# Optimization experiments

Hardware: AMD Instinct MI355X
Metric: run time of the kernel (lower is better)

## Reference

```python
import jax, jax.numpy as jnp
import numpy as np

B, E, N1, K, CIN, CB, COUT, G = 2, 2048, 96, 32, 64, 32, 64, 4
NEG_SLOPE = 0.01  # nn.LeakyReLU default


def setup_inputs() -> dict:
    key = jax.random.key(0)
    ks = jax.random.split(key, 9)
    sites1 = jax.random.normal(ks[0], (B, N1, CIN), jnp.float32)
    sites2 = jax.random.normal(ks[1], (B, K, CIN), jnp.float32)
    bonds = jax.random.normal(ks[2], (B, E, CB), jnp.float32)
    idx1 = jax.random.randint(ks[3], (E,), 0, N1, jnp.int32)
    idx2 = jax.random.randint(ks[4], (E,), 0, K, jnp.int32)
    idx2_oh = jax.nn.one_hot(idx2, K, dtype=jnp.float32)  # [E, K]
    F = 2 * CIN + CB
    W_eq = jax.random.normal(ks[5], (G, F, COUT), jnp.float32) / np.float32(np.sqrt(F))
    b_eq = jnp.zeros((COUT,), jnp.float32)
    W_att = jax.random.normal(ks[6], (COUT, 1), jnp.float32) / np.float32(np.sqrt(COUT))
    b_att = jnp.zeros((1,), jnp.float32)
    # permutation group action on the K cells: identity + random perms
    perms = [jnp.arange(K, dtype=jnp.int32)]
    pk = ks[7]
    for _ in range(G - 1):
        pk, sk = jax.random.split(pk)
        perms.append(jax.random.permutation(sk, K).astype(jnp.int32))
    perms1 = jnp.stack(perms)  # [G, K]
    perms2 = perms1            # same action on input and output cell axes
    return dict(sites1=sites1, sites2=sites2, bonds=bonds, W_eq=W_eq, b_eq=b_eq,
                W_att=W_att, b_att=b_att, idx2_oh=idx2_oh, idx1=idx1, idx2=idx2,
                perms1=perms1, perms2=perms2)


def reference(sites1, sites2, bonds, W_eq, b_eq, W_att, b_att, idx2_oh, idx1, idx2, perms1, perms2):
    Bn = sites1.shape[0]
    Gn, Kn = perms1.shape
    On = W_eq.shape[2]
    # gather sender / receiver site features along the site axis
    sites_s = jnp.take(sites1, idx1, axis=1)              # [B,E,CIN]
    sites_r = jnp.take(sites2, idx2, axis=1)              # [B,E,CIN]
    vectors = jnp.concatenate([sites_s, sites_r, bonds], axis=2)  # [B,E,F]
    # outer-product expansion onto cells (idx2_oh is one-hot over K)
    vc = jnp.einsum('bef,ek->befk', vectors, idx2_oh)     # [B,E,F,K]
    # permutation-equivariant linear (group-averaged): per-group-element weight,
    # input cells permuted by perms1, output cells un-permuted by perms2
    xg = vc[:, :, :, perms1]                               # [B,E,F,G,K]
    yg = jnp.einsum('befgk,gfo->beogk', xg, W_eq)          # [B,E,O,G,K]
    inv2 = jnp.argsort(perms2, axis=1)                     # inverse perms [G,K]
    garr = jnp.arange(Gn)[:, None]
    y = yg[:, :, :, garr, inv2].mean(axis=3)               # [B,E,O,K]
    y = jax.nn.leaky_relu(y + b_eq[None, None, :, None], NEG_SLOPE)
    # gather each edge's receiving cell slot == dot with one-hot
    lat = jnp.einsum('beok,ek->beo', y, idx2_oh)           # [B,E,O]
    att = jax.nn.sigmoid(jnp.einsum('beo,oj->bej', lat, W_att) + b_att)  # [B,E,1]
    lat = att * lat
    # scatter_add over edges into receiving sites
    out = jnp.zeros((Bn, Kn, On), lat.dtype).at[:, idx2].add(lat)  # [B,K,O]
    return out
```

## Files before the change

### kernel.cpp

```cpp
#include <hip/hip_runtime.h>
#include <math.h>

#define Bn   2
#define En   2048
#define N1n  96
#define Kn   32
#define CINn 64
#define CBn  32
#define On   64
#define Gn   4
#define Fn   160
#define NEG  0.01f
#define NW   8
#define NT   (NW * 64)
#define EB   2
#define SUBn 8
#define ELCAP 128

__global__ void __launch_bounds__(NT, 4)
fused_kernel(const float* __restrict__ sites1, const float* __restrict__ sites2,
             const float* __restrict__ bonds,  const float* __restrict__ W_eq,
             const float* __restrict__ b_eq,   const float* __restrict__ W_att,
             const float* __restrict__ b_att,  const int* __restrict__ idx1,
             const int* __restrict__ idx2,     const int* __restrict__ perms1,
             const int* __restrict__ perms2,   float* __restrict__ ws) {
    __shared__ float Weff[Fn][On];
    __shared__ float vs[NW][EB][96];
    __shared__ float red[NW][On];
    __shared__ float s2[CINn];
    __shared__ float wgs[Gn];
    __shared__ int   elist[ELCAP];
    __shared__ int   ecount;

    const int t      = threadIdx.x;
    const int bucket = blockIdx.x >> 3;
    const int sub    = blockIdx.x & (SUBn - 1);
    const int b      = bucket >> 5;
    const int k2     = bucket & (Kn - 1);

    if (t < Gn) wgs[t] = 0.f;
    __builtin_amdgcn_wave_barrier();
    if (t < 64) {
        const int pa2 = perms2[t],      pa1 = perms1[t];
        const int pb2 = perms2[t + 64], pb1 = perms1[t + 64];
        if (pa2 == k2 && pa1 == k2) wgs[t >> 5] = 1.f;
        if (pb2 == k2 && pb1 == k2) wgs[(t + 64) >> 5] = 1.f;
    }
    if (t == 64) ecount = 0;
    __syncthreads();

    for (int e = t; e < En; e += NT)
        if (idx2[e] == k2 && (e & (SUBn - 1)) == sub) {
            int p = atomicAdd(&ecount, 1);
            elist[p] = e;
        }

    {
        const float w0 = wgs[0], w1 = wgs[1], w2 = wgs[2], w3 = wgs[3];
        const float4* W4 = (const float4*)W_eq;
        float4* Wd = (float4*)&Weff[0][0];
        const int n4 = Fn * On / 4;
#pragma unroll
        for (int i = t; i < n4; i += NT) {
            float4 a0 = W4[i], a1 = W4[n4 + i], a2 = W4[2 * n4 + i], a3 = W4[3 * n4 + i];
            float4 r;
            r.x = 0.25f * (w0 * a0.x + w1 * a1.x + w2 * a2.x + w3 * a3.x);
            r.y = 0.25f * (w0 * a0.y + w1 * a1.y + w2 * a2.y + w3 * a3.y);
            r.z = 0.25f * (w0 * a0.z + w1 * a1.z + w2 * a2.z + w3 * a3.z);
            r.w = 0.25f * (w0 * a0.w + w1 * a1.w + w2 * a2.w + w3 * a3.w);
            Wd[i] = r;
        }
    }

    if (t < CINn) s2[t] = sites2[(b * Kn + k2) * CINn + t];
    __syncthreads();

    const int w    = t >> 6;
    const int lane = t & 63;
    const int og   = lane & 15;
    const int fg   = lane >> 4;
    const int ec   = ecount;

    const float4 be4 = ((const float4*)b_eq)[og];
    const float4 wa  = ((const float4*)W_att)[og];
    const float  ba  = b_att[0];

    float4 p2 = make_float4(0.f, 0.f, 0.f, 0.f);
#pragma unroll
    for (int fi = 0; fi < 16; ++fi) {
        const int f  = 64 + 4 * fi + fg;
        const float  vf = s2[4 * fi + fg];
        const float4 wv = *(const float4*)&Weff[f][og * 4];
        p2.x += vf * wv.x; p2.y += vf * wv.y;
        p2.z += vf * wv.z; p2.w += vf * wv.w;
    }

    float4 oacc = make_float4(0.f, 0.f, 0.f, 0.f);

    for (int base = w * EB; base < ec; base += NW * EB) {
        const int nb = (ec - base < EB) ? (ec - base) : EB;

        __builtin_amdgcn_wave_barrier();
#pragma unroll
        for (int j = 0; j < EB; ++j) {
            const int jj = j < nb ? j : nb - 1;
            const int e  = elist[base + jj];
            const int i1 = idx1[e];
            vs[w][j][lane] = sites1[((b * N1n + i1) << 6) + lane];
            if (lane < CBn) vs[w][j][CINn + lane] = bonds[(b * En + e) * CBn + lane];
        }
        __builtin_amdgcn_wave_barrier();

        float4 acc[EB];
#pragma unroll
        for (int j = 0; j < EB; ++j) acc[j] = p2;

#pragma unroll
        for (int fi = 0; fi < 24; ++fi) {
            const int vsidx = 4 * fi + fg;
            const int f     = vsidx < CINn ? vsidx : vsidx + CINn;
            const float4 wv = *(const float4*)&Weff[f][og * 4];
#pragma unroll
            for (int j = 0; j < EB; ++j) {
                const float vf = vs[w][j][vsidx];
                acc[j].x += vf * wv.x; acc[j].y += vf * wv.y;
                acc[j].z += vf * wv.z; acc[j].w += vf * wv.w;
            }
        }
        __builtin_amdgcn_wave_barrier();

#pragma unroll
        for (int j = 0; j < EB; ++j) {
            float4 a = acc[j];
#pragma unroll
            for (int m = 16; m <= 32; m <<= 1) {
                a.x += __shfl_xor(a.x, m);
                a.y += __shfl_xor(a.y, m);
                a.z += __shfl_xor(a.z, m);
                a.w += __shfl_xor(a.w, m);
            }
            float4 lat;
            lat.x = a.x + be4.x; lat.x = lat.x > 0.f ? lat.x : NEG * lat.x;
            lat.y = a.y + be4.y; lat.y = lat.y > 0.f ? lat.y : NEG * lat.y;
            lat.z = a.z + be4.z; lat.z = lat.z > 0.f ? lat.z : NEG * lat.z;
            lat.w = a.w + be4.w; lat.w = lat.w > 0.f ? lat.w : NEG * lat.w;

            float part = lat.x * wa.x + lat.y * wa.y + lat.z * wa.z + lat.w * wa.w;
#pragma unroll
            for (int m = 1; m <= 8; m <<= 1) part += __shfl_xor(part, m);

            float att = 1.f / (1.f + expf(-(part + ba)));
            att *= (j < nb) ? 1.f : 0.f;
            oacc.x += att * lat.x;
            oacc.y += att * lat.y;
            oacc.z += att * lat.z;
            oacc.w += att * lat.w;
        }
    }

    if (fg == 0) *(float4*)&red[w][og * 4] = oacc;
    __syncthreads();

    if (t < On) {
        float s = 0.f;
#pragma unroll
        for (int q = 0; q < NW; ++q) s += red[q][t];
        ws[((size_t)bucket * SUBn + sub) * On + t] = s;
    }
}

__global__ void __launch_bounds__(256)
reduce_kernel(const float* __restrict__ ws, float* __restrict__ out) {
    const int i = blockIdx.x * 256 + threadIdx.x;
    const int bucket = i >> 6;
    const int o      = i & (On - 1);
    const float* p = ws + (size_t)bucket * SUBn * On + o;
    float s01 = p[0]      + p[On];
    float s23 = p[2 * On] + p[3 * On];
    float s45 = p[4 * On] + p[5 * On];
    float s67 = p[6 * On] + p[7 * On];
    out[i] = (s01 + s23) + (s45 + s67);
}

extern "C" void kernel_launch(void* const* d_in, const int* in_sizes, int n_in,
                              void* d_out, int out_size, void* d_ws, size_t ws_size,
                              hipStream_t stream) {
    const float* sites1 = (const float*)d_in[0];
    const float* sites2 = (const float*)d_in[1];
    const float* bonds  = (const float*)d_in[2];
    const float* W_eq   = (const float*)d_in[3];
    const float* b_eq   = (const float*)d_in[4];
    const float* W_att  = (const float*)d_in[5];
    const float* b_att  = (const float*)d_in[6];
    const int*   idx1   = (const int*)d_in[8];
    const int*   idx2   = (const int*)d_in[9];
    const int*   perms1 = (const int*)d_in[10];
    const int*   perms2 = (const int*)d_in[11];
    float* out = (float*)d_out;
    float* ws  = (float*)d_ws;

    fused_kernel<<<Bn * Kn * SUBn, NT, 0, stream>>>(
        sites1, sites2, bonds, W_eq, b_eq, W_att, b_att,
        idx1, idx2, perms1, perms2, ws);
    reduce_kernel<<<(Bn * Kn * On) / 256, 256, 0, stream>>>(ws, out);
}
```

Baseline: 84.58 us.

## Precompute per-cell weights and edge lists in prep kernel; fuse final reduction via ticket

A new prep kernel builds the group-averaged weight matrix once per receiving cell, rather than once in every one of the 512 blocks, and builds each cell's edge list once in global workspace. The main kernel copies the precomputed weights into shared memory and takes a contiguous slice of the edge list. The separate reduce kernel is replaced by a last-block-done atomic ticket that sums the partials inside the main kernel. This removes redundant W_eq reads and per-block idx2 scans at the cost of an extra launch and workspace traffic. Two risks: edges beyond 160 per cell are dropped, and the ticket counters are reset only for t<64, which covers all 64 buckets.

```diff
diff --git a/kernel.cpp b/kernel.cpp
--- a/kernel.cpp
+++ b/kernel.cpp
@@ -15,53 +15,40 @@
 #define NT   (NW * 64)
 #define EB   2
 #define SUBn 8
-#define ELCAP 128
-
-__global__ void __launch_bounds__(NT, 4)
-fused_kernel(const float* __restrict__ sites1, const float* __restrict__ sites2,
-             const float* __restrict__ bonds,  const float* __restrict__ W_eq,
-             const float* __restrict__ b_eq,   const float* __restrict__ W_att,
-             const float* __restrict__ b_att,  const int* __restrict__ idx1,
-             const int* __restrict__ idx2,     const int* __restrict__ perms1,
-             const int* __restrict__ perms2,   float* __restrict__ ws) {
-    __shared__ float Weff[Fn][On];
-    __shared__ float vs[NW][EB][96];
-    __shared__ float red[NW][On];
-    __shared__ float s2[CINn];
-    __shared__ float wgs[Gn];
-    __shared__ int   elist[ELCAP];
-    __shared__ int   ecount;
-
-    const int t      = threadIdx.x;
-    const int bucket = blockIdx.x >> 3;
-    const int sub    = blockIdx.x & (SUBn - 1);
-    const int b      = bucket >> 5;
-    const int k2     = bucket & (Kn - 1);
-
-    if (t < Gn) wgs[t] = 0.f;
-    __builtin_amdgcn_wave_barrier();
-    if (t < 64) {
-        const int pa2 = perms2[t],      pa1 = perms1[t];
-        const int pb2 = perms2[t + 64], pb1 = perms1[t + 64];
-        if (pa2 == k2 && pa1 == k2) wgs[t >> 5] = 1.f;
-        if (pb2 == k2 && pb1 == k2) wgs[(t + 64) >> 5] = 1.f;
-    }
-    if (t == 64) ecount = 0;
-    __syncthreads();
-
-    for (int e = t; e < En; e += NT)
-        if (idx2[e] == k2 && (e & (SUBn - 1)) == sub) {
-            int p = atomicAdd(&ecount, 1);
-            elist[p] = e;
-        }
-
-    {
+#define LCAP 160
+
+#define WS_TICK 0
+#define WS_CNT  64
+#define WS_LIST 256
+#define WS_WEFF 8192
+#define WS_PART (8192 + 32 * Fn * On)
+
+__global__ void __launch_bounds__(NT)
+prep_kernel(const float* __restrict__ W_eq, const int* __restrict__ perms1,
+            const int* __restrict__ perms2, const int* __restrict__ idx2,
+            float* __restrict__ wsf) {
+    int* wsi = (int*)wsf;
+    const int t    = threadIdx.x;
+    const int role = blockIdx.x;
+
+    if (role < 64) {
+        const int k2 = role >> 1;
+        __shared__ float wgs[Gn];
+        if (t < Gn) wgs[t] = 0.f;
+        __builtin_amdgcn_wave_barrier();
+        if (t < 64) {
+            const int pa2 = perms2[t],      pa1 = perms1[t];
+            const int pb2 = perms2[t + 64], pb1 = perms1[t + 64];
+            if (pa2 == k2 && pa1 == k2) wgs[t >> 5] = 1.f;
+            if (pb2 == k2 && pb1 == k2) wgs[(t + 64) >> 5] = 1.f;
+        }
+        __syncthreads();
         const float w0 = wgs[0], w1 = wgs[1], w2 = wgs[2], w3 = wgs[3];
         const float4* W4 = (const float4*)W_eq;
-        float4* Wd = (float4*)&Weff[0][0];
+        float4* Wd = (float4*)(wsf + WS_WEFF + k2 * (Fn * On));
         const int n4 = Fn * On / 4;
-#pragma unroll
-        for (int i = t; i < n4; i += NT) {
+        const int i0 = (role & 1) * (n4 / 2);
+        for (int i = i0 + t; i < i0 + n4 / 2; i += NT) {
             float4 a0 = W4[i], a1 = W4[n4 + i], a2 = W4[2 * n4 + i], a3 = W4[3 * n4 + i];
             float4 r;
             r.x = 0.25f * (w0 * a0.x + w1 * a1.x + w2 * a2.x + w3 * a3.x);
@@ -70,8 +57,54 @@
             r.w = 0.25f * (w0 * a0.w + w1 * a1.w + w2 * a2.w + w3 * a3.w);
             Wd[i] = r;
         }
-    }
-
+    } else {
+        const int k2 = role - 64;
+        __shared__ int cntS;
+        if (t == 0) cntS = 0;
+        if (role == 64 && t < 64) wsi[WS_TICK + t] = 0;
+        __syncthreads();
+        for (int e = t; e < En; e += NT)
+            if (idx2[e] == k2) {
+                int p = atomicAdd(&cntS, 1);
+                if (p < LCAP) wsi[WS_LIST + k2 * LCAP + p] = e;
+            }
+        __syncthreads();
+        if (t == 0) wsi[WS_CNT + k2] = cntS < LCAP ? cntS : LCAP;
+    }
+}
+
+__global__ void __launch_bounds__(NT, 4)
+fused_kernel(const float* __restrict__ sites1, const float* __restrict__ sites2,
+             const float* __restrict__ bonds,  const float* __restrict__ b_eq,
+             const float* __restrict__ W_att,  const float* __restrict__ b_att,
+             const int* __restrict__ idx1,     float* __restrict__ wsf,
+             float* __restrict__ out) {
+    __shared__ float Weff[Fn][On];
+    __shared__ float vs[NW][EB][96];
+    __shared__ float red[NW][On];
+    __shared__ float s2[CINn];
+    __shared__ int   el[64];
+    __shared__ int   s_last;
+
+    int* wsi = (int*)wsf;
+    const int t      = threadIdx.x;
+    const int bucket = blockIdx.x >> 3;
+    const int sub    = blockIdx.x & (SUBn - 1);
+    const int b      = bucket >> 5;
+    const int k2     = bucket & (Kn - 1);
+
+    const int c  = wsi[WS_CNT + k2];
+    const int ch = (c + SUBn - 1) >> 3;
+    const int lo = sub * ch;
+    int n = c - lo; if (n > ch) n = ch; if (n < 0) n = 0;
+    if (t < n) el[t] = wsi[WS_LIST + k2 * LCAP + lo + t];
+
+    {
+        const float4* Ws4 = (const float4*)(wsf + WS_WEFF + k2 * (Fn * On));
+        float4* Wd = (float4*)&Weff[0][0];
+#pragma unroll
+        for (int i = t; i < Fn * On / 4; i += NT) Wd[i] = Ws4[i];
+    }
     if (t < CINn) s2[t] = sites2[(b * Kn + k2) * CINn + t];
     __syncthreads();
 
@@ -79,7 +112,6 @@
     const int lane = t & 63;
     const int og   = lane & 15;
     const int fg   = lane >> 4;
-    const int ec   = ecount;
 
     const float4 be4 = ((const float4*)b_eq)[og];
     const float4 wa  = ((const float4*)W_att)[og];
@@ -97,14 +129,14 @@
 
     float4 oacc = make_float4(0.f, 0.f, 0.f, 0.f);
 
-    for (int base = w * EB; base < ec; base += NW * EB) {
-        const int nb = (ec - base < EB) ? (ec - base) : EB;
+    for (int base = w * EB; base < n; base += NW * EB) {
+        const int nb = (n - base < EB) ? (n - base) : EB;
 
         __builtin_amdgcn_wave_barrier();
 #pragma unroll
         for (int j = 0; j < EB; ++j) {
             const int jj = j < nb ? j : nb - 1;
-            const int e  = elist[base + jj];
+            const int e  = el[base + jj];
             const int i1 = idx1[e];
             vs[w][j][lane] = sites1[((b * N1n + i1) << 6) + lane];
             if (lane < CBn) vs[w][j][CINn + lane] = bonds[(b * En + e) * CBn + lane];
@@ -165,21 +197,26 @@
         float s = 0.f;
 #pragma unroll
         for (int q = 0; q < NW; ++q) s += red[q][t];
-        ws[((size_t)bucket * SUBn + sub) * On + t] = s;
-    }
-}
-
-__global__ void __launch_bounds__(256)
-reduce_kernel(const float* __restrict__ ws, float* __restrict__ out) {
-    const int i = blockIdx.x * 256 + threadIdx.x;
-    const int bucket = i >> 6;
-    const int o      = i & (On - 1);
-    const float* p = ws + (size_t)bucket * SUBn * On + o;
-    float s01 = p[0]      + p[On];
-    float s23 = p[2 * On] + p[3 * On];
-    float s45 = p[4 * On] + p[5 * On];
-    float s67 = p[6 * On] + p[7 * On];
-    out[i] = (s01 + s23) + (s45 + s67);
+        wsf[WS_PART + ((size_t)bucket * SUBn + sub) * On + t] = s;
+    }
+    __syncthreads();
+
+    if (t == 0) {
+        __threadfence();
+        int old = atomicAdd(&wsi[WS_TICK + bucket], 1);
+        int last = (old == SUBn - 1);
+        if (last) __threadfence();
+        s_last = last;
+    }
+    __syncthreads();
+    if (s_last && t < On) {
+        const float* p = wsf + WS_PART + (size_t)bucket * SUBn * On + t;
+        float s01 = p[0]      + p[On];
+        float s23 = p[2 * On] + p[3 * On];
+        float s45 = p[4 * On] + p[5 * On];
+        float s67 = p[6 * On] + p[7 * On];
+        out[bucket * On + t] = (s01 + s23) + (s45 + s67);
+    }
 }
 
 extern "C" void kernel_launch(void* const* d_in, const int* in_sizes, int n_in,
@@ -197,10 +234,9 @@
     const int*   perms1 = (const int*)d_in[10];
     const int*   perms2 = (const int*)d_in[11];
     float* out = (float*)d_out;
-    float* ws  = (float*)d_ws;
-
+    float* wsf = (float*)d_ws;
+
+    prep_kernel<<<96, NT, 0, stream>>>(W_eq, perms1, perms2, idx2, wsf);
     fused_kernel<<<Bn * Kn * SUBn, NT, 0, stream>>>(
-        sites1, sites2, bonds, W_eq, b_eq, W_att, b_att,
-        idx1, idx2, perms1, perms2, ws);
-    reduce_kernel<<<(Bn * Kn * On) / 256, 256, 0, stream>>>(ws, out);
+        sites1, sites2, bonds, b_eq, W_att, b_att, idx1, wsf, out);
 }
```

Measured after the change: 95.98 us. 13.5% more time.
